# Optimization experiments

Hardware: AMD Instinct MI355X
Metric: run time of the kernel (lower is better)

The kernel has to match this reference:

```python
import jax, jax.numpy as jnp
import numpy as np

DIM = 1024
HEADS = 16

def setup_inputs() -> dict:
    key = jax.random.key(0)
    k1, k2, k3, k4 = jax.random.split(key, 4)
    x = jax.random.normal(k1, (2, 2048, DIM), dtype=jnp.float32)
    ln_gamma = jnp.ones((DIM,), dtype=jnp.float32)
    ln_beta = jnp.zeros((DIM,), dtype=jnp.float32)
    # torch Linear weight is [out, in]; store transposed [in, out] for x @ W
    W_qkv = jax.random.normal(k2, (DIM, 3 * DIM), dtype=jnp.float32) * (DIM ** -0.5)
    W_out = jax.random.normal(k3, (DIM, DIM), dtype=jnp.float32) * (DIM ** -0.5)
    b_out = jax.random.normal(k4, (DIM,), dtype=jnp.float32) * 0.02
    return {"x": x, "ln_gamma": ln_gamma, "ln_beta": ln_beta,
            "W_qkv": W_qkv, "W_out": W_out, "b_out": b_out}

def reference(x, ln_gamma, ln_beta, W_qkv, W_out, b_out):
    B, N, C = x.shape
    H = HEADS
    Dh = C // H
    scale = Dh ** -0.5
    # LayerNorm (eps=1e-5, torch default)
    mu = jnp.mean(x, axis=-1, keepdims=True)
    var = jnp.var(x, axis=-1, keepdims=True)
    xn = (x - mu) / jnp.sqrt(var + 1e-5) * ln_gamma + ln_beta
    # QKV projection: [B,N,3C] -> [3,B,H,N,Dh]
    qkv = (xn @ W_qkv).reshape(B, N, 3, H, Dh).transpose(2, 0, 3, 1, 4)
    q, k, v = qkv[0], qkv[1], qkv[2]
    attn = jnp.einsum('bhnd,bhmd->bhnm', q, k) * scale  # [B,H,N,N]
    attn = jax.nn.softmax(attn, axis=-1)
    out = jnp.einsum('bhnm,bhmd->bhnd', attn, v)  # [B,H,N,Dh]
    out = out.transpose(0, 2, 1, 3).reshape(B, N, C)
    return out @ W_out + b_out
```

## Files before the change

kernel.cpp:

```cpp
#include <hip/hip_runtime.h>
#include <hip/hip_bf16.h>

#define DIM 1024
#define HEADS 16
#define DH 64
#define SEQ 2048
#define BATCH 2
#define ROWS (BATCH*SEQ)
#define C3 (3*DIM)

typedef __attribute__((ext_vector_type(8))) short s16x8;
typedef __attribute__((ext_vector_type(4))) float f32x4;
typedef __attribute__((ext_vector_type(16))) float f32x16;
typedef __attribute__((ext_vector_type(4))) unsigned int u32x4;

__device__ __forceinline__ void gll16(const void* g, void* l) {
  __builtin_amdgcn_global_load_lds((const __attribute__((address_space(1))) void*)g,
                                   (__attribute__((address_space(3))) void*)l, 16, 0, 0);
}
__device__ __forceinline__ float bf2f(short s) {
  return __builtin_bit_cast(float, ((unsigned)(unsigned short)s) << 16);
}
__device__ __forceinline__ short f2bf(float f) {
  return (short)__bfloat16_as_ushort(__float2bfloat16(f));
}
__device__ __forceinline__ unsigned pk2(float a, float b) {
  unsigned lo = (unsigned)__bfloat16_as_ushort(__float2bfloat16(a));
  unsigned hh = (unsigned)__bfloat16_as_ushort(__float2bfloat16(b));
  return lo | (hh << 16);
}
__device__ __forceinline__ float fexp2(float x) {
#if __has_builtin(__builtin_amdgcn_exp2f)
  return __builtin_amdgcn_exp2f(x);
#else
  float r; asm("v_exp_f32 %0, %1" : "=v"(r) : "v"(x)); return r;
#endif
}

__global__ __launch_bounds__(256) void ln_kernel(const float* __restrict__ x,
    const float* __restrict__ gamma, const float* __restrict__ beta,
    __hip_bfloat16* __restrict__ xn) {
  int row = blockIdx.x;
  int t = threadIdx.x;
  const float4* xp = (const float4*)(x + (size_t)row * DIM);
  float4 v = xp[t];
  float s = v.x + v.y + v.z + v.w;
  float q = v.x*v.x + v.y*v.y + v.z*v.z + v.w*v.w;
  for (int off = 32; off >= 1; off >>= 1) {
    s += __shfl_xor(s, off, 64);
    q += __shfl_xor(q, off, 64);
  }
  __shared__ float red[8];
  int w = t >> 6;
  if ((t & 63) == 0) { red[w] = s; red[4 + w] = q; }
  __syncthreads();
  s = red[0] + red[1] + red[2] + red[3];
  q = red[4] + red[5] + red[6] + red[7];
  float mu = s * (1.0f / DIM);
  float var = q * (1.0f / DIM) - mu * mu;
  float rstd = rsqrtf(var + 1e-5f);
  int c = t * 4;
  float4 g4 = ((const float4*)gamma)[t];
  float4 b4 = ((const float4*)beta)[t];
  __hip_bfloat16* op = xn + (size_t)row * DIM + c;
  op[0] = __float2bfloat16((v.x - mu) * rstd * g4.x + b4.x);
  op[1] = __float2bfloat16((v.y - mu) * rstd * g4.y + b4.y);
  op[2] = __float2bfloat16((v.z - mu) * rstd * g4.z + b4.z);
  op[3] = __float2bfloat16((v.w - mu) * rstd * g4.w + b4.w);
}

__global__ __launch_bounds__(256) void transpose_cvt(const float* __restrict__ in,
    __hip_bfloat16* __restrict__ out, int R, int Cn) {
  __shared__ float tile[32][33];
  int c0 = blockIdx.x * 32, r0 = blockIdx.y * 32;
  int tx = threadIdx.x & 31, ty = threadIdx.x >> 5;
#pragma unroll
  for (int i = 0; i < 4; i++)
    tile[ty + i * 8][tx] = in[(size_t)(r0 + ty + i * 8) * Cn + c0 + tx];
  __syncthreads();
#pragma unroll
  for (int i = 0; i < 4; i++)
    out[(size_t)(c0 + ty + i * 8) * R + r0 + tx] = __float2bfloat16(tile[tx][ty + i * 8]);
}

template<int WITH_BIAS, int BN>
__global__ __launch_bounds__(256) void gemm_bt(const __hip_bfloat16* __restrict__ A,
    const __hip_bfloat16* __restrict__ Bt, void* __restrict__ Cptr,
    const float* __restrict__ bias, int M, int Nc, int K) {
  constexpr int NB = BN / 32;
  __shared__ short lds_a[128 * 32];
  __shared__ short lds_b[BN * 32];
  int t = threadIdx.x;
  int l = t & 63, w = t >> 6;
  int wr = w >> 1, wc = w & 1;
  int m0 = blockIdx.y * 128, n0 = blockIdx.x * BN;
  f32x4 acc[4][NB] = {};
  const short* Ab = (const short*)A;
  const short* Bb = (const short*)Bt;
  int srow = t >> 2;
  int scol = (t & 3) * 8;
  char* la = (char*)lds_a + (t >> 6) * 1024;
  char* lb = (char*)lds_b + (t >> 6) * 1024;
  for (int kk = 0; kk < K; kk += 32) {
    gll16(Ab + (size_t)(m0 + srow) * K + kk + scol,      la);
    gll16(Ab + (size_t)(m0 + 64 + srow) * K + kk + scol, la + 4096);
    gll16(Bb + (size_t)(n0 + srow) * K + kk + scol,      lb);
    if (BN == 128)
      gll16(Bb + (size_t)(n0 + 64 + srow) * K + kk + scol, lb + 4096);
    asm volatile("s_waitcnt vmcnt(0)" ::: "memory");
    __syncthreads();
    s16x8 af[4], bf[NB];
#pragma unroll
    for (int m = 0; m < 4; m++)
      af[m] = *(const s16x8*)&lds_a[(wr * 64 + m * 16 + (l & 15)) * 32 + (l >> 4) * 8];
#pragma unroll
    for (int n = 0; n < NB; n++)
      bf[n] = *(const s16x8*)&lds_b[(wc * (BN / 2) + n * 16 + (l & 15)) * 32 + (l >> 4) * 8];
#pragma unroll
    for (int m = 0; m < 4; m++)
#pragma unroll
      for (int n = 0; n < NB; n++)
        acc[m][n] = __builtin_amdgcn_mfma_f32_16x16x32_bf16(af[m], bf[n], acc[m][n], 0, 0, 0);
    __syncthreads();
  }
  if (WITH_BIAS) {
    float* C = (float*)Cptr;
#pragma unroll
    for (int m = 0; m < 4; m++)
#pragma unroll
      for (int n = 0; n < NB; n++) {
        int col = n0 + wc * (BN / 2) + n * 16 + (l & 15);
        float bb = bias[col];
#pragma unroll
        for (int r = 0; r < 4; r++) {
          int row = m0 + wr * 64 + m * 16 + (l >> 4) * 4 + r;
          C[(size_t)row * Nc + col] = acc[m][n][r] + bb;
        }
      }
  } else {
    __hip_bfloat16* C = (__hip_bfloat16*)Cptr;
#pragma unroll
    for (int m = 0; m < 4; m++)
#pragma unroll
      for (int n = 0; n < NB; n++) {
        int col = n0 + wc * (BN / 2) + n * 16 + (l & 15);
#pragma unroll
        for (int r = 0; r < 4; r++) {
          int row = m0 + wr * 64 + m * 16 + (l >> 4) * 4 + r;
          C[(size_t)row * Nc + col] = __float2bfloat16(acc[m][n][r]);
        }
      }
  }
}

__global__ __launch_bounds__(256) void attn_kernel(const __hip_bfloat16* __restrict__ qkv,
    __hip_bfloat16* __restrict__ attno) {
  const int t = threadIdx.x, l = t & 63, w = t >> 6;
  const int hi = l >> 5, lq = l & 31;
  const int qb = blockIdx.x, bh = blockIdx.y;
  const int b = bh >> 4, h = bh & 15;
  const short* base  = (const short*)qkv + (size_t)b * SEQ * C3 + h * DH;
  const short* kbase = base + DIM;
  const short* vbase = base + 2 * DIM;
  const int qr0 = qb * 128 + w * 32;

  __shared__ short kbuf[2][64 * 64];
  __shared__ short vbuf[2][64 * 64];

  const float SCL = 0.125f * 1.44269504089f;
  s16x8 qf[4];
#pragma unroll
  for (int dk = 0; dk < 4; dk++) {
    s16x8 raw = *(const s16x8*)(base + (size_t)(qr0 + lq) * C3 + dk * 16 + hi * 8);
#pragma unroll
    for (int j = 0; j < 8; j++) qf[dk][j] = f2bf(bf2f(raw[j]) * SCL);
  }

  s16x8 ones;
#pragma unroll
  for (int j = 0; j < 8; j++) ones[j] = (short)0x3F80;

  f32x16 o0, o1, osum;
#pragma unroll
  for (int r = 0; r < 16; r++) { o0[r] = 0.f; o1[r] = 0.f; osum[r] = 0.f; }

  const int krow = t >> 3, kchk = t & 7;
  const int ksrc = kchk ^ (krow & 7);
  const int vr = t & 31, vc = (t >> 5) * 8;

  {
    char* kd = (char*)&kbuf[0][0];
    gll16(kbase + (size_t)krow * C3 + ksrc * 8,        kd + t * 16);
    gll16(kbase + (size_t)(32 + krow) * C3 + ksrc * 8, kd + 4096 + t * 16);
    u32x4 vau = __builtin_bit_cast(u32x4, *(const s16x8*)(vbase + (size_t)(2 * vr) * C3 + vc));
    u32x4 vbu = __builtin_bit_cast(u32x4, *(const s16x8*)(vbase + (size_t)(2 * vr + 1) * C3 + vc));
    char* vd = (char*)&vbuf[0][0];
#pragma unroll
    for (int i = 0; i < 8; i++) {
      unsigned dw = __builtin_amdgcn_perm(vbu[i >> 1], vau[i >> 1],
                                          (i & 1) ? 0x07060302u : 0x05040100u);
      *(unsigned*)(vd + (vc + i) * 128 + (((vr >> 2) ^ i) * 16) + (vr & 3) * 4) = dw;
    }
  }
  __syncthreads();

  for (int tile = 0; tile < SEQ / 64; ++tile) {
    const int cur = tile & 1;
    const bool pf = (tile + 1 < SEQ / 64);
    u32x4 vau, vbu;
    if (pf) {
      const int kv1 = (tile + 1) * 64;
      char* kd = (char*)&kbuf[cur ^ 1][0];
      gll16(kbase + (size_t)(kv1 + krow) * C3 + ksrc * 8,      kd + t * 16);
      gll16(kbase + (size_t)(kv1 + 32 + krow) * C3 + ksrc * 8, kd + 4096 + t * 16);
      vau = __builtin_bit_cast(u32x4, *(const s16x8*)(vbase + (size_t)(kv1 + 2 * vr) * C3 + vc));
      vbu = __builtin_bit_cast(u32x4, *(const s16x8*)(vbase + (size_t)(kv1 + 2 * vr + 1) * C3 + vc));
    }
    const char* kb = (const char*)&kbuf[cur][0];
    f32x16 st0, st1;
#pragma unroll
    for (int r = 0; r < 16; r++) { st0[r] = 0.f; st1[r] = 0.f; }
#pragma unroll
    for (int dk = 0; dk < 4; dk++) {
      int chk = ((2 * dk + hi) ^ (l & 7)) * 16;
      s16x8 kf0 = *(const s16x8*)(kb + (size_t)lq * 128 + chk);
      s16x8 kf1 = *(const s16x8*)(kb + (size_t)(32 + lq) * 128 + chk);
      st0 = __builtin_amdgcn_mfma_f32_32x32x16_bf16(kf0, qf[dk], st0, 0, 0, 0);
      st1 = __builtin_amdgcn_mfma_f32_32x32x16_bf16(kf1, qf[dk], st1, 0, 0, 0);
    }
#pragma unroll
    for (int r = 0; r < 16; r++) {
      st0[r] = fexp2(st0[r]);
      st1[r] = fexp2(st1[r]);
    }
    const char* vbp = (const char*)&vbuf[cur][0];
#pragma unroll
    for (int n = 0; n < 2; n++) {
      const f32x16& stn = n ? st1 : st0;
#pragma unroll
      for (int ksl = 0; ksl < 2; ksl++) {
        int rb = ksl * 8;
        int a  = (int)pk2(stn[rb + 0], stn[rb + 1]);
        int bq = (int)pk2(stn[rb + 2], stn[rb + 3]);
        int c  = (int)pk2(stn[rb + 4], stn[rb + 5]);
        int d  = (int)pk2(stn[rb + 6], stn[rb + 7]);
        asm volatile("v_permlane32_swap_b32 %0, %1" : "+v"(a), "+v"(c));
        asm volatile("v_permlane32_swap_b32 %0, %1" : "+v"(bq), "+v"(d));
        u32x4 fr;
        fr.x = (unsigned)a;  fr.y = (unsigned)bq;
        fr.z = (unsigned)c;  fr.w = (unsigned)d;
        s16x8 pa = __builtin_bit_cast(s16x8, fr);
        int ks = n * 2 + ksl;
        int chk = ((2 * ks + hi) ^ (l & 7)) * 16;
        s16x8 vf0 = *(const s16x8*)(vbp + (size_t)lq * 128 + chk);
        s16x8 vf1 = *(const s16x8*)(vbp + (size_t)(32 + lq) * 128 + chk);
        o0   = __builtin_amdgcn_mfma_f32_32x32x16_bf16(pa, vf0, o0, 0, 0, 0);
        o1   = __builtin_amdgcn_mfma_f32_32x32x16_bf16(pa, vf1, o1, 0, 0, 0);
        osum = __builtin_amdgcn_mfma_f32_32x32x16_bf16(pa, ones, osum, 0, 0, 0);
      }
    }
    if (pf) {
      char* vd = (char*)&vbuf[cur ^ 1][0];
#pragma unroll
      for (int i = 0; i < 8; i++) {
        unsigned dw = __builtin_amdgcn_perm(vbu[i >> 1], vau[i >> 1],
                                            (i & 1) ? 0x07060302u : 0x05040100u);
        *(unsigned*)(vd + (vc + i) * 128 + (((vr >> 2) ^ i) * 16) + (vr & 3) * 4) = dw;
      }
    }
    __syncthreads();
  }
#pragma unroll
  for (int r = 0; r < 16; r++) {
    int qr = (r & 3) + 8 * (r >> 2) + 4 * hi;
    float ir = 1.0f / osum[r];
    size_t rowoff = (size_t)(b * SEQ + qr0 + qr) * DIM + h * DH;
    attno[rowoff + lq]      = __float2bfloat16(o0[r] * ir);
    attno[rowoff + 32 + lq] = __float2bfloat16(o1[r] * ir);
  }
}

extern "C" void kernel_launch(void* const* d_in, const int* in_sizes, int n_in,
                              void* d_out, int out_size, void* d_ws, size_t ws_size,
                              hipStream_t stream) {
  const float* x     = (const float*)d_in[0];
  const float* gamma = (const float*)d_in[1];
  const float* beta  = (const float*)d_in[2];
  const float* Wqkv  = (const float*)d_in[3];
  const float* Wout  = (const float*)d_in[4];
  const float* bout  = (const float*)d_in[5];

  __hip_bfloat16* xn     = (__hip_bfloat16*)d_ws;
  __hip_bfloat16* wqkv_t = xn + (size_t)ROWS * DIM;
  __hip_bfloat16* wout_t = wqkv_t + (size_t)C3 * DIM;
  __hip_bfloat16* qkv    = wout_t + (size_t)DIM * DIM;
  __hip_bfloat16* attno  = qkv + (size_t)ROWS * C3;

  ln_kernel<<<ROWS, 256, 0, stream>>>(x, gamma, beta, xn);
  transpose_cvt<<<dim3(C3 / 32, DIM / 32), 256, 0, stream>>>(Wqkv, wqkv_t, DIM, C3);
  transpose_cvt<<<dim3(DIM / 32, DIM / 32), 256, 0, stream>>>(Wout, wout_t, DIM, DIM);
  gemm_bt<0, 128><<<dim3(C3 / 128, ROWS / 128), 256, 0, stream>>>(xn, wqkv_t, (void*)qkv, nullptr, ROWS, C3, DIM);
  attn_kernel<<<dim3(SEQ / 128, BATCH * HEADS), 256, 0, stream>>>(qkv, attno);
  gemm_bt<1, 64><<<dim3(DIM / 64, ROWS / 128), 256, 0, stream>>>(attno, wout_t, d_out, bout, ROWS, DIM, DIM);
}
```

Baseline: 129.7 us.

## Add 256x256 QKV GEMM kernel and widen attention blocks to 512 threads

Adds a new 512-thread GEMM for the QKV projection. It uses 256x256 output tiles, K-step 64, swizzled LDS, double-buffered global_load_lds prefetch and 16x16x32 MFMAs, which raises operand reuse per LDS load. The attention kernel now processes 256 query rows per block with 8 waves, so each K/V tile staged in LDS is shared by twice as many queries. Each thread loads half as much K/V per tile. The cost is larger LDS use (128KB for the GEMM) and fewer blocks (192 GEMM blocks, 256 attention blocks), which may underfill the 256 CUs.

```diff
diff --git a/kernel.cpp b/kernel.cpp
--- a/kernel.cpp
+++ b/kernel.cpp
@@ -10,9 +10,11 @@
 #define C3 (3*DIM)
 
 typedef __attribute__((ext_vector_type(8))) short s16x8;
+typedef __attribute__((ext_vector_type(4))) short s16x4;
 typedef __attribute__((ext_vector_type(4))) float f32x4;
 typedef __attribute__((ext_vector_type(16))) float f32x16;
 typedef __attribute__((ext_vector_type(4))) unsigned int u32x4;
+typedef __attribute__((ext_vector_type(2))) unsigned int u32x2;
 
 __device__ __forceinline__ void gll16(const void* g, void* l) {
   __builtin_amdgcn_global_load_lds((const __attribute__((address_space(1))) void*)g,
@@ -81,6 +83,83 @@
 #pragma unroll
   for (int i = 0; i < 4; i++)
     out[(size_t)(c0 + ty + i * 8) * R + r0 + tx] = __float2bfloat16(tile[tx][ty + i * 8]);
+}
+
+__global__ __launch_bounds__(512) void gemm256(const __hip_bfloat16* __restrict__ A,
+    const __hip_bfloat16* __restrict__ Bt, __hip_bfloat16* __restrict__ C,
+    int M, int Nc, int K) {
+  __shared__ short lds[2][2][256 * 64];
+  const int t = threadIdx.x, l = t & 63;
+  const int w = t >> 6, wr = w >> 2, wc = w & 3;
+  const int m0 = blockIdx.y * 256, n0 = blockIdx.x * 256;
+  const short* Ab = (const short*)A;
+  const short* Bb = (const short*)Bt;
+  f32x4 acc[8][4] = {};
+  const int srow = t >> 3;
+  const int schk = (t & 7) ^ (srow & 7);
+  const int NIT = K / 64;
+
+  {
+    char* la = (char*)&lds[0][0][0];
+    char* lb = (char*)&lds[0][1][0];
+#pragma unroll
+    for (int p = 0; p < 4; p++) {
+      gll16(Ab + (size_t)(m0 + p * 64 + srow) * K + schk * 8, la + p * 8192 + t * 16);
+      gll16(Bb + (size_t)(n0 + p * 64 + srow) * K + schk * 8, lb + p * 8192 + t * 16);
+    }
+  }
+  for (int it = 0; it < NIT; ++it) {
+    const int cur = it & 1;
+    __syncthreads();
+    if (it + 1 < NIT) {
+      const int kk = (it + 1) * 64;
+      char* la = (char*)&lds[cur ^ 1][0][0];
+      char* lb = (char*)&lds[cur ^ 1][1][0];
+#pragma unroll
+      for (int p = 0; p < 4; p++) {
+        gll16(Ab + (size_t)(m0 + p * 64 + srow) * K + kk + schk * 8, la + p * 8192 + t * 16);
+        gll16(Bb + (size_t)(n0 + p * 64 + srow) * K + kk + schk * 8, lb + p * 8192 + t * 16);
+      }
+      asm volatile("s_waitcnt vmcnt(8)" ::: "memory");
+    } else {
+      asm volatile("s_waitcnt vmcnt(0)" ::: "memory");
+    }
+    __syncthreads();
+    const char* la = (const char*)&lds[cur][0][0];
+    const char* lb = (const char*)&lds[cur][1][0];
+#pragma unroll
+    for (int s = 0; s < 2; s++) {
+      s16x8 af[8], bf[4];
+#pragma unroll
+      for (int f = 0; f < 8; f++) {
+        int row = wr * 128 + f * 16 + (l & 15);
+        int chk = ((s * 4 + (l >> 4)) ^ (l & 7)) * 16;
+        af[f] = *(const s16x8*)(la + row * 128 + chk);
+      }
+#pragma unroll
+      for (int n = 0; n < 4; n++) {
+        int row = wc * 64 + n * 16 + (l & 15);
+        int chk = ((s * 4 + (l >> 4)) ^ (l & 7)) * 16;
+        bf[n] = *(const s16x8*)(lb + row * 128 + chk);
+      }
+#pragma unroll
+      for (int f = 0; f < 8; f++)
+#pragma unroll
+        for (int n = 0; n < 4; n++)
+          acc[f][n] = __builtin_amdgcn_mfma_f32_16x16x32_bf16(af[f], bf[n], acc[f][n], 0, 0, 0);
+    }
+  }
+#pragma unroll
+  for (int f = 0; f < 8; f++)
+#pragma unroll
+    for (int n = 0; n < 4; n++) {
+      int col = n0 + wc * 64 + n * 16 + (l & 15);
+#pragma unroll
+      for (int r = 0; r < 4; r++) {
+        int row = m0 + wr * 128 + f * 16 + (l >> 4) * 4 + r;
+        C[(size_t)row * Nc + col] = __float2bfloat16(acc[f][n][r]);
+      }
+    }
 }
 
 template<int WITH_BIAS, int BN>
@@ -153,7 +232,7 @@
   }
 }
 
-__global__ __launch_bounds__(256) void attn_kernel(const __hip_bfloat16* __restrict__ qkv,
+__global__ __launch_bounds__(512) void attn_kernel(const __hip_bfloat16* __restrict__ qkv,
     __hip_bfloat16* __restrict__ attno) {
   const int t = threadIdx.x, l = t & 63, w = t >> 6;
   const int hi = l >> 5, lq = l & 31;
@@ -162,7 +241,7 @@
   const short* base  = (const short*)qkv + (size_t)b * SEQ * C3 + h * DH;
   const short* kbase = base + DIM;
   const short* vbase = base + 2 * DIM;
-  const int qr0 = qb * 128 + w * 32;
+  const int qr0 = qb * 256 + w * 32;
 
   __shared__ short kbuf[2][64 * 64];
   __shared__ short vbuf[2][64 * 64];
@@ -184,22 +263,21 @@
 #pragma unroll
   for (int r = 0; r < 16; r++) { o0[r] = 0.f; o1[r] = 0.f; osum[r] = 0.f; }
 
-  const int krow = t >> 3, kchk = t & 7;
-  const int ksrc = kchk ^ (krow & 7);
-  const int vr = t & 31, vc = (t >> 5) * 8;
+  const int krow = t >> 3;
+  const int ksrc = (t & 7) ^ (krow & 7);
+  const int vr = t & 31, vcg = t >> 5;
 
   {
-    char* kd = (char*)&kbuf[0][0];
-    gll16(kbase + (size_t)krow * C3 + ksrc * 8,        kd + t * 16);
-    gll16(kbase + (size_t)(32 + krow) * C3 + ksrc * 8, kd + 4096 + t * 16);
-    u32x4 vau = __builtin_bit_cast(u32x4, *(const s16x8*)(vbase + (size_t)(2 * vr) * C3 + vc));
-    u32x4 vbu = __builtin_bit_cast(u32x4, *(const s16x8*)(vbase + (size_t)(2 * vr + 1) * C3 + vc));
+    gll16(kbase + (size_t)krow * C3 + ksrc * 8, (char*)&kbuf[0][0] + t * 16);
+    u32x2 vau = __builtin_bit_cast(u32x2, *(const s16x4*)(vbase + (size_t)(2 * vr) * C3 + vcg * 4));
+    u32x2 vbu = __builtin_bit_cast(u32x2, *(const s16x4*)(vbase + (size_t)(2 * vr + 1) * C3 + vcg * 4));
     char* vd = (char*)&vbuf[0][0];
 #pragma unroll
-    for (int i = 0; i < 8; i++) {
+    for (int i = 0; i < 4; i++) {
+      int d = vcg * 4 + i;
       unsigned dw = __builtin_amdgcn_perm(vbu[i >> 1], vau[i >> 1],
                                           (i & 1) ? 0x07060302u : 0x05040100u);
-      *(unsigned*)(vd + (vc + i) * 128 + (((vr >> 2) ^ i) * 16) + (vr & 3) * 4) = dw;
+      *(unsigned*)(vd + d * 128 + (((vr >> 2) ^ (d & 7)) * 16) + (vr & 3) * 4) = dw;
     }
   }
   __syncthreads();
@@ -207,14 +285,12 @@
   for (int tile = 0; tile < SEQ / 64; ++tile) {
     const int cur = tile & 1;
     const bool pf = (tile + 1 < SEQ / 64);
-    u32x4 vau, vbu;
+    u32x2 vau, vbu;
     if (pf) {
       const int kv1 = (tile + 1) * 64;
-      char* kd = (char*)&kbuf[cur ^ 1][0];
-      gll16(kbase + (size_t)(kv1 + krow) * C3 + ksrc * 8,      kd + t * 16);
-      gll16(kbase + (size_t)(kv1 + 32 + krow) * C3 + ksrc * 8, kd + 4096 + t * 16);
-      vau = __builtin_bit_cast(u32x4, *(const s16x8*)(vbase + (size_t)(kv1 + 2 * vr) * C3 + vc));
-      vbu = __builtin_bit_cast(u32x4, *(const s16x8*)(vbase + (size_t)(kv1 + 2 * vr + 1) * C3 + vc));
+      gll16(kbase + (size_t)(kv1 + krow) * C3 + ksrc * 8, (char*)&kbuf[cur ^ 1][0] + t * 16);
+      vau = __builtin_bit_cast(u32x2, *(const s16x4*)(vbase + (size_t)(kv1 + 2 * vr) * C3 + vcg * 4));
+      vbu = __builtin_bit_cast(u32x2, *(const s16x4*)(vbase + (size_t)(kv1 + 2 * vr + 1) * C3 + vcg * 4));
     }
     const char* kb = (const char*)&kbuf[cur][0];
     f32x16 st0, st1;
@@ -262,10 +338,11 @@
     if (pf) {
       char* vd = (char*)&vbuf[cur ^ 1][0];
 #pragma unroll
-      for (int i = 0; i < 8; i++) {
+      for (int i = 0; i < 4; i++) {
+        int d = vcg * 4 + i;
         unsigned dw = __builtin_amdgcn_perm(vbu[i >> 1], vau[i >> 1],
                                             (i & 1) ? 0x07060302u : 0x05040100u);
-        *(unsigned*)(vd + (vc + i) * 128 + (((vr >> 2) ^ i) * 16) + (vr & 3) * 4) = dw;
+        *(unsigned*)(vd + d * 128 + (((vr >> 2) ^ (d & 7)) * 16) + (vr & 3) * 4) = dw;
       }
     }
     __syncthreads();
@@ -299,7 +376,7 @@
   ln_kernel<<<ROWS, 256, 0, stream>>>(x, gamma, beta, xn);
   transpose_cvt<<<dim3(C3 / 32, DIM / 32), 256, 0, stream>>>(Wqkv, wqkv_t, DIM, C3);
   transpose_cvt<<<dim3(DIM / 32, DIM / 32), 256, 0, stream>>>(Wout, wout_t, DIM, DIM);
-  gemm_bt<0, 128><<<dim3(C3 / 128, ROWS / 128), 256, 0, stream>>>(xn, wqkv_t, (void*)qkv, nullptr, ROWS, C3, DIM);
-  attn_kernel<<<dim3(SEQ / 128, BATCH * HEADS), 256, 0, stream>>>(qkv, attno);
+  gemm256<<<dim3(C3 / 256, ROWS / 256), 512, 0, stream>>>(xn, wqkv_t, qkv, ROWS, C3, DIM);
+  attn_kernel<<<dim3(SEQ / 256, BATCH * HEADS), 512, 0, stream>>>(qkv, attno);
   gemm_bt<1, 64><<<dim3(DIM / 64, ROWS / 128), 256, 0, stream>>>(attno, wout_t, d_out, bout, ROWS, DIM, DIM);
 }
```

Result: no change. 130.2 us (+0.4%).
